# Kernel tuning notes

Measured on AMD Instinct MI355X. Metric: run time of the kernel, lower is better.

## Reference

```python
import jax, jax.numpy as jnp
import numpy as np

B_SZ, L, D, N = 2, 2048, 1024, 16


def setup_inputs() -> dict:
    key = jax.random.key(0)
    ks = jax.random.split(key, 8)
    x = jax.random.normal(ks[0], (B_SZ, L, D), dtype=jnp.float32)
    # torch.nn.Linear params: weight [out, in], bias [out]; y = x @ W.T + b
    s1 = 1.0 / np.sqrt(D)
    W1 = jax.random.uniform(ks[1], (D, D), minval=-s1, maxval=s1, dtype=jnp.float32)
    b1 = jax.random.uniform(ks[2], (D,), minval=-s1, maxval=s1, dtype=jnp.float32)
    W2 = jax.random.uniform(ks[3], (N, D), minval=-s1, maxval=s1, dtype=jnp.float32)
    b2 = jax.random.uniform(ks[4], (N,), minval=-s1, maxval=s1, dtype=jnp.float32)
    W3 = jax.random.uniform(ks[5], (N, D), minval=-s1, maxval=s1, dtype=jnp.float32)
    b3 = jax.random.uniform(ks[6], (N,), minval=-s1, maxval=s1, dtype=jnp.float32)
    # A: xavier_uniform on (D, N)
    lim = np.sqrt(6.0 / (D + N))
    A = jax.random.uniform(ks[7], (D, N), minval=-lim, maxval=lim, dtype=jnp.float32)
    return {"x": x, "W1": W1, "b1": b1, "W2": W2, "b2": b2, "W3": W3, "b3": b3, "A": A}


def reference(x, W1, b1, W2, b2, W3, b3, A):
    # delta = softplus(fc1(x)); B = fc2(x); C = fc3(x)
    delta = jax.nn.softplus(x @ W1.T + b1)          # [b, l, d]
    Bm = x @ W2.T + b2                               # [b, l, n]
    Cm = x @ W3.T + b3                               # [b, l, n]
    # discretization: dB = einsum('bld,bln->bldn', delta, B)
    dB = jnp.einsum('bld,bln->bldn', delta, Bm)      # [b, l, d, n]
    # dA = exp(einsum('bld,dn->bldn', delta, A)) is computed in the source but
    # multiplies a zero-initialized h, so it does not affect the output.
    # h = dA*0 + x[..., None] * dB
    h = x[..., None] * dB                            # [b, l, d, n]
    y = jnp.einsum('bln,bldn->bld', Cm, h)           # [b, l, d]
    return y
```

## Files before the change

kernel.cpp:

```cpp
#include <hip/hip_runtime.h>
#include <hip/hip_bf16.h>
#include <math.h>


typedef __bf16 bf16x8 __attribute__((ext_vector_type(8)));
typedef __bf16 bf16x4 __attribute__((ext_vector_type(4)));
typedef float  f32x4  __attribute__((ext_vector_type(4)));

#define MDIM 4096
#define KDIM 1024
#define NDIM 1024

__device__ __forceinline__ void async16(const void* g, void* l) {
    __builtin_amdgcn_global_load_lds(
        (const __attribute__((address_space(1))) void*)g,
        (__attribute__((address_space(3))) void*)l, 16, 0, 0);
}

__device__ __forceinline__ float softplus_f(float z) {
    return fmaxf(z, 0.f) + log1pf(__expf(-fabsf(z)));
}

#define NX4 ((MDIM * KDIM) / 4)
#define NW4 ((KDIM * NDIM) / 4)
__global__ __launch_bounds__(256)
void convert_kernel(const float* __restrict__ x, const float* __restrict__ W1,
                    __bf16* __restrict__ xb, __bf16* __restrict__ w1b) {
    int i = blockIdx.x * 256 + threadIdx.x;
    if (i < NX4) {
        float4 v = reinterpret_cast<const float4*>(x)[i];
        bf16x4 h = { (__bf16)v.x, (__bf16)v.y, (__bf16)v.z, (__bf16)v.w };
        reinterpret_cast<bf16x4*>(xb)[i] = h;
    } else {
        int j = i - NX4;
        float4 v = reinterpret_cast<const float4*>(W1)[j];
        bf16x4 h = { (__bf16)v.x, (__bf16)v.y, (__bf16)v.z, (__bf16)v.w };
        reinterpret_cast<bf16x4*>(w1b)[j] = h;
    }
}

__global__ __launch_bounds__(256)
void s_kernel_mfma(const __bf16* __restrict__ xb,
                   const float* __restrict__ W2, const float* __restrict__ b2,
                   const float* __restrict__ W3, const float* __restrict__ b3,
                   float* __restrict__ s) {
    __shared__ __align__(16) __bf16 As[64 * 64];
    __shared__ __align__(16) __bf16 Ws[32 * 64];
    const int t = threadIdx.x;
    const int wave = t >> 6, lane = t & 63;
    const int lrow = lane & 15, quad = lane >> 4;
    const int srow = lane >> 3, scol = (lane & 7) * 8;
    const size_t m0 = (size_t)blockIdx.x * 64;

    const int wrow = t >> 3;
    const int wcol = (t & 7) * 8;
    const float* __restrict__ wsrc =
        (wrow < 16) ? (W2 + (size_t)wrow * KDIM) : (W3 + (size_t)(wrow - 16) * KDIM);

    f32x4 acc[2] = {};

    for (int k0 = 0; k0 < KDIM; k0 += 64) {
#pragma unroll
        for (int i = 0; i < 2; ++i) {
            int q = i * 4 + wave;
            int row = 8 * q + srow;
            async16(xb + (m0 + row) * KDIM + k0 + scol, &As[q * 512]);
        }
        {
            float4 v0 = *reinterpret_cast<const float4*>(wsrc + k0 + wcol);
            float4 v1 = *reinterpret_cast<const float4*>(wsrc + k0 + wcol + 4);
            bf16x8 h = { (__bf16)v0.x, (__bf16)v0.y, (__bf16)v0.z, (__bf16)v0.w,
                         (__bf16)v1.x, (__bf16)v1.y, (__bf16)v1.z, (__bf16)v1.w };
            *reinterpret_cast<bf16x8*>(&Ws[wrow * 64 + wcol]) = h;
        }
        __syncthreads();
#pragma unroll
        for (int kk = 0; kk < 64; kk += 32) {
            bf16x8 a = *reinterpret_cast<const bf16x8*>(
                &As[(wave * 16 + lrow) * 64 + kk + quad * 8]);
#pragma unroll
            for (int ni = 0; ni < 2; ++ni) {
                bf16x8 b = *reinterpret_cast<const bf16x8*>(
                    &Ws[(ni * 16 + lrow) * 64 + kk + quad * 8]);
                acc[ni] = __builtin_amdgcn_mfma_f32_16x16x32_bf16(a, b, acc[ni], 0, 0, 0);
            }
        }
        __syncthreads();
    }

    const float b2v = b2[lrow], b3v = b3[lrow];
#pragma unroll
    for (int r = 0; r < 4; ++r) {
        float p = (acc[0][r] + b2v) * (acc[1][r] + b3v);
        p += __shfl_xor(p, 1);
        p += __shfl_xor(p, 2);
        p += __shfl_xor(p, 4);
        p += __shfl_xor(p, 8);
        if (lrow == 0) s[m0 + wave * 16 + quad * 4 + r] = p;
    }
}

#define GBM 128
#define GBN 128
#define GBK 64
__global__ __launch_bounds__(256)
void gemm_bf(const __bf16* __restrict__ xb, const __bf16* __restrict__ w1b,
             const float* __restrict__ x, const float* __restrict__ b1,
             const float* __restrict__ s, float* __restrict__ y) {
    __shared__ __align__(16) __bf16 As[GBM * GBK];
    __shared__ __align__(16) __bf16 Bs[GBN * GBK];
    const int bm = blockIdx.y, bn = blockIdx.x;
    const int t = threadIdx.x;
    const int wave = t >> 6, lane = t & 63;
    const int wm = (wave >> 1) * 64, wn = (wave & 1) * 64;
    const int lrow = lane & 15, quad = lane >> 4;
    const int srow = lane >> 3, scol = (lane & 7) * 8;
    const size_t m0 = (size_t)bm * GBM, n0 = (size_t)bn * GBN;

    f32x4 acc[4][4] = {};

    for (int k0 = 0; k0 < KDIM; k0 += GBK) {
#pragma unroll
        for (int i = 0; i < 4; ++i) {
            int q = i * 4 + wave;
            int row = 8 * q + srow;
            async16(xb  + (m0 + row) * KDIM + k0 + scol, &As[q * 512]);
            async16(w1b + (n0 + row) * KDIM + k0 + scol, &Bs[q * 512]);
        }
        __syncthreads();
#pragma unroll
        for (int kk = 0; kk < GBK; kk += 32) {
            bf16x8 af[4], bfr[4];
#pragma unroll
            for (int mi = 0; mi < 4; ++mi)
                af[mi] = *reinterpret_cast<const bf16x8*>(
                    &As[(wm + mi * 16 + lrow) * GBK + kk + quad * 8]);
#pragma unroll
            for (int ni = 0; ni < 4; ++ni)
                bfr[ni] = *reinterpret_cast<const bf16x8*>(
                    &Bs[(wn + ni * 16 + lrow) * GBK + kk + quad * 8]);
#pragma unroll
            for (int mi = 0; mi < 4; ++mi)
#pragma unroll
                for (int ni = 0; ni < 4; ++ni)
                    acc[mi][ni] = __builtin_amdgcn_mfma_f32_16x16x32_bf16(
                        af[mi], bfr[ni], acc[mi][ni], 0, 0, 0);
        }
        __syncthreads();
    }

#pragma unroll
    for (int ni = 0; ni < 4; ++ni) {
        const size_t gn = n0 + wn + ni * 16 + lrow;
        const float bias = b1[gn];
#pragma unroll
        for (int mi = 0; mi < 4; ++mi) {
#pragma unroll
            for (int r = 0; r < 4; ++r) {
                const size_t gm = m0 + wm + mi * 16 + quad * 4 + r;
                float z = acc[mi][ni][r] + bias;
                y[gm * NDIM + gn] = x[gm * NDIM + gn] * softplus_f(z) * s[gm];
            }
        }
    }
}

__global__ __launch_bounds__(256)
void s_kernel_fb(const float* __restrict__ x,
                 const float* __restrict__ W2, const float* __restrict__ b2,
                 const float* __restrict__ W3, const float* __restrict__ b3,
                 float* __restrict__ s) {
    __shared__ float xs[1024];
    __shared__ float ps[8][32];
    __shared__ float bc[32];
    const int m = blockIdx.x;
    const int t = threadIdx.x;
    reinterpret_cast<float4*>(xs)[t] =
        reinterpret_cast<const float4*>(x + (size_t)m * 1024)[t];
    __syncthreads();
    const int n = t & 15;
    const int mat = (t >> 4) & 1;
    const int seg = t >> 5;
    const float* __restrict__ W = mat ? W3 : W2;
    const float* __restrict__ wr = W + (size_t)n * 1024 + seg * 128;
    const float* __restrict__ xr = xs + seg * 128;
    float p = 0.f;
#pragma unroll
    for (int i = 0; i < 128; i += 4) {
        float4 w4 = *reinterpret_cast<const float4*>(wr + i);
        float4 x4 = *reinterpret_cast<const float4*>(xr + i);
        p += w4.x * x4.x + w4.y * x4.y + w4.z * x4.z + w4.w * x4.w;
    }
    ps[seg][t & 31] = p;
    __syncthreads();
    if (t < 32) {
        float tot = 0.f;
#pragma unroll
        for (int g = 0; g < 8; ++g) tot += ps[g][t];
        tot += (t < 16) ? b2[t] : b3[t - 16];
        bc[t] = tot;
    }
    __syncthreads();
    if (t == 0) {
        float ss = 0.f;
#pragma unroll
        for (int nn = 0; nn < 16; ++nn) ss += bc[nn] * bc[16 + nn];
        s[m] = ss;
    }
}

#define BM 128
#define BN 64
#define BK 64
#define LDK 72
__global__ __launch_bounds__(256)
void gemm_fused_fb(const float* __restrict__ x, const float* __restrict__ W1,
                   const float* __restrict__ b1, const float* __restrict__ s,
                   float* __restrict__ y) {
    __shared__ __align__(16) __bf16 As[BM * LDK];
    __shared__ __align__(16) __bf16 Bs[BN * LDK];
    const int bm = blockIdx.y;
    const int bn = blockIdx.x;
    const int t = threadIdx.x;
    const int wave = t >> 6;
    const int lane = t & 63;
    const int wm = (wave >> 1) * 64;
    const int wn = (wave & 1) * 32;
    const int lrow = lane & 15;
    const int quad = lane >> 4;
    f32x4 acc[4][2] = {};
    const int rbase = t >> 4;
    const int scol = (t & 15) * 4;
    const float* __restrict__ xg = x + (size_t)(bm * BM) * KDIM + scol;
    const float* __restrict__ wg = W1 + (size_t)(bn * BN) * KDIM + scol;
    for (int k0 = 0; k0 < KDIM; k0 += BK) {
#pragma unroll
        for (int rr = 0; rr < 8; ++rr) {
            int row = rr * 16 + rbase;
            float4 v = *reinterpret_cast<const float4*>(xg + (size_t)row * KDIM + k0);
            bf16x4 h = { (__bf16)v.x, (__bf16)v.y, (__bf16)v.z, (__bf16)v.w };
            *reinterpret_cast<bf16x4*>(&As[row * LDK + scol]) = h;
        }
#pragma unroll
        for (int rr = 0; rr < 4; ++rr) {
            int row = rr * 16 + rbase;
            float4 v = *reinterpret_cast<const float4*>(wg + (size_t)row * KDIM + k0);
            bf16x4 h = { (__bf16)v.x, (__bf16)v.y, (__bf16)v.z, (__bf16)v.w };
            *reinterpret_cast<bf16x4*>(&Bs[row * LDK + scol]) = h;
        }
        __syncthreads();
#pragma unroll
        for (int kk = 0; kk < BK; kk += 32) {
            bf16x8 af[4];
            bf16x8 bfr[2];
#pragma unroll
            for (int mi = 0; mi < 4; ++mi)
                af[mi] = *reinterpret_cast<const bf16x8*>(
                    &As[(wm + mi * 16 + lrow) * LDK + kk + quad * 8]);
#pragma unroll
            for (int ni = 0; ni < 2; ++ni)
                bfr[ni] = *reinterpret_cast<const bf16x8*>(
                    &Bs[(wn + ni * 16 + lrow) * LDK + kk + quad * 8]);
#pragma unroll
            for (int mi = 0; mi < 4; ++mi)
#pragma unroll
                for (int ni = 0; ni < 2; ++ni)
                    acc[mi][ni] = __builtin_amdgcn_mfma_f32_16x16x32_bf16(
                        af[mi], bfr[ni], acc[mi][ni], 0, 0, 0);
        }
        __syncthreads();
    }
    const int gmb = bm * BM + wm;
    const int gnb = bn * BN + wn;
#pragma unroll
    for (int ni = 0; ni < 2; ++ni) {
        const int gn = gnb + ni * 16 + lrow;
        const float bias = b1[gn];
#pragma unroll
        for (int mi = 0; mi < 4; ++mi) {
            const int gm0 = gmb + mi * 16 + quad * 4;
#pragma unroll
            for (int r = 0; r < 4; ++r) {
                const int gm = gm0 + r;
                float z = acc[mi][ni][r] + bias;
                y[(size_t)gm * NDIM + gn] =
                    x[(size_t)gm * NDIM + gn] * softplus_f(z) * s[gm];
            }
        }
    }
}

extern "C" void kernel_launch(void* const* d_in, const int* in_sizes, int n_in,
                              void* d_out, int out_size, void* d_ws, size_t ws_size,
                              hipStream_t stream) {
    const float* x  = (const float*)d_in[0];
    const float* W1 = (const float*)d_in[1];
    const float* b1 = (const float*)d_in[2];
    const float* W2 = (const float*)d_in[3];
    const float* b2 = (const float*)d_in[4];
    const float* W3 = (const float*)d_in[5];
    const float* b3 = (const float*)d_in[6];

    float* y = (float*)d_out;

    const size_t XB_BYTES = (size_t)MDIM * KDIM * 2;
    const size_t WB_BYTES = (size_t)NDIM * KDIM * 2;
    const size_t S_BYTES  = (size_t)MDIM * 4;

    if (ws_size >= XB_BYTES + WB_BYTES + S_BYTES) {
        __bf16* xb  = (__bf16*)d_ws;
        __bf16* w1b = (__bf16*)((char*)d_ws + XB_BYTES);
        float*  s   = (float*)((char*)d_ws + XB_BYTES + WB_BYTES);
        convert_kernel<<<dim3((NX4 + NW4) / 256), dim3(256), 0, stream>>>(x, W1, xb, w1b);
        s_kernel_mfma<<<dim3(MDIM / 64), dim3(256), 0, stream>>>(xb, W2, b2, W3, b3, s);
        gemm_bf<<<dim3(NDIM / GBN, MDIM / GBM), dim3(256), 0, stream>>>(xb, w1b, x, b1, s, y);
    } else {
        float* s = (float*)d_ws;
        s_kernel_fb<<<dim3(MDIM), dim3(256), 0, stream>>>(x, W2, b2, W3, b3, s);
        gemm_fused_fb<<<dim3(NDIM / BN, MDIM / BM), dim3(256), 0, stream>>>(x, W1, b1, s, y);
    }
}
```

Measured before the change: 135.4 us.

## Fuse conversion and s-projection into one prep kernel; swizzle LDS and shrink GEMM tile

Result: faster. 114.0 us (-15.8%).

```diff
diff --git a/kernel.cpp b/kernel.cpp
--- a/kernel.cpp
+++ b/kernel.cpp
@@ -21,87 +21,86 @@
     return fmaxf(z, 0.f) + log1pf(__expf(-fabsf(z)));
 }
 
-#define NX4 ((MDIM * KDIM) / 4)
-#define NW4 ((KDIM * NDIM) / 4)
 __global__ __launch_bounds__(256)
-void convert_kernel(const float* __restrict__ x, const float* __restrict__ W1,
-                    __bf16* __restrict__ xb, __bf16* __restrict__ w1b) {
-    int i = blockIdx.x * 256 + threadIdx.x;
-    if (i < NX4) {
-        float4 v = reinterpret_cast<const float4*>(x)[i];
-        bf16x4 h = { (__bf16)v.x, (__bf16)v.y, (__bf16)v.z, (__bf16)v.w };
-        reinterpret_cast<bf16x4*>(xb)[i] = h;
-    } else {
-        int j = i - NX4;
-        float4 v = reinterpret_cast<const float4*>(W1)[j];
-        bf16x4 h = { (__bf16)v.x, (__bf16)v.y, (__bf16)v.z, (__bf16)v.w };
-        reinterpret_cast<bf16x4*>(w1b)[j] = h;
-    }
-}
-
-__global__ __launch_bounds__(256)
-void s_kernel_mfma(const __bf16* __restrict__ xb,
-                   const float* __restrict__ W2, const float* __restrict__ b2,
-                   const float* __restrict__ W3, const float* __restrict__ b3,
-                   float* __restrict__ s) {
-    __shared__ __align__(16) __bf16 As[64 * 64];
-    __shared__ __align__(16) __bf16 Ws[32 * 64];
+void prep_kernel(const float* __restrict__ x, const float* __restrict__ W1,
+                 const float* __restrict__ W2, const float* __restrict__ b2,
+                 const float* __restrict__ W3, const float* __restrict__ b3,
+                 __bf16* __restrict__ xb, __bf16* __restrict__ w1b,
+                 float* __restrict__ s) {
+    __shared__ __align__(16) __bf16 xs[16 * 1032];
+    __shared__ float red[4][2][16][16];
     const int t = threadIdx.x;
     const int wave = t >> 6, lane = t & 63;
     const int lrow = lane & 15, quad = lane >> 4;
-    const int srow = lane >> 3, scol = (lane & 7) * 8;
-    const size_t m0 = (size_t)blockIdx.x * 64;
-
-    const int wrow = t >> 3;
-    const int wcol = (t & 7) * 8;
-    const float* __restrict__ wsrc =
-        (wrow < 16) ? (W2 + (size_t)wrow * KDIM) : (W3 + (size_t)(wrow - 16) * KDIM);
+    const size_t m0 = (size_t)blockIdx.x * 16;
+
+    {
+        const float4* src = reinterpret_cast<const float4*>(W1) + (size_t)blockIdx.x * 1024;
+        bf16x4* dst = reinterpret_cast<bf16x4*>(w1b) + (size_t)blockIdx.x * 1024;
+#pragma unroll
+        for (int i = 0; i < 4; ++i) {
+            float4 v = src[i * 256 + t];
+            bf16x4 h = { (__bf16)v.x, (__bf16)v.y, (__bf16)v.z, (__bf16)v.w };
+            dst[i * 256 + t] = h;
+        }
+    }
+
+#pragma unroll
+    for (int i = 0; i < 16; ++i) {
+        float4 v = *reinterpret_cast<const float4*>(x + (m0 + i) * KDIM + t * 4);
+        bf16x4 h = { (__bf16)v.x, (__bf16)v.y, (__bf16)v.z, (__bf16)v.w };
+        *reinterpret_cast<bf16x4*>(&xs[i * 1032 + t * 4]) = h;
+        *reinterpret_cast<bf16x4*>(xb + (m0 + i) * KDIM + t * 4) = h;
+    }
+    __syncthreads();
 
     f32x4 acc[2] = {};
-
-    for (int k0 = 0; k0 < KDIM; k0 += 64) {
-#pragma unroll
-        for (int i = 0; i < 2; ++i) {
-            int q = i * 4 + wave;
-            int row = 8 * q + srow;
-            async16(xb + (m0 + row) * KDIM + k0 + scol, &As[q * 512]);
-        }
+    const int wk0 = wave * 256;
+#pragma unroll
+    for (int ks = 0; ks < 256; ks += 32) {
+        bf16x8 a = *reinterpret_cast<const bf16x8*>(
+            &xs[lrow * 1032 + wk0 + ks + quad * 8]);
         {
-            float4 v0 = *reinterpret_cast<const float4*>(wsrc + k0 + wcol);
-            float4 v1 = *reinterpret_cast<const float4*>(wsrc + k0 + wcol + 4);
-            bf16x8 h = { (__bf16)v0.x, (__bf16)v0.y, (__bf16)v0.z, (__bf16)v0.w,
+            const float* wp = W2 + (size_t)lrow * KDIM + wk0 + ks + quad * 8;
+            float4 v0 = *reinterpret_cast<const float4*>(wp);
+            float4 v1 = *reinterpret_cast<const float4*>(wp + 4);
+            bf16x8 b = { (__bf16)v0.x, (__bf16)v0.y, (__bf16)v0.z, (__bf16)v0.w,
                          (__bf16)v1.x, (__bf16)v1.y, (__bf16)v1.z, (__bf16)v1.w };
-            *reinterpret_cast<bf16x8*>(&Ws[wrow * 64 + wcol]) = h;
-        }
-        __syncthreads();
-#pragma unroll
-        for (int kk = 0; kk < 64; kk += 32) {
-            bf16x8 a = *reinterpret_cast<const bf16x8*>(
-                &As[(wave * 16 + lrow) * 64 + kk + quad * 8]);
-#pragma unroll
-            for (int ni = 0; ni < 2; ++ni) {
-                bf16x8 b = *reinterpret_cast<const bf16x8*>(
-                    &Ws[(ni * 16 + lrow) * 64 + kk + quad * 8]);
-                acc[ni] = __builtin_amdgcn_mfma_f32_16x16x32_bf16(a, b, acc[ni], 0, 0, 0);
-            }
-        }
-        __syncthreads();
-    }
-
-    const float b2v = b2[lrow], b3v = b3[lrow];
+            acc[0] = __builtin_amdgcn_mfma_f32_16x16x32_bf16(a, b, acc[0], 0, 0, 0);
+        }
+        {
+            const float* wp = W3 + (size_t)lrow * KDIM + wk0 + ks + quad * 8;
+            float4 v0 = *reinterpret_cast<const float4*>(wp);
+            float4 v1 = *reinterpret_cast<const float4*>(wp + 4);
+            bf16x8 b = { (__bf16)v0.x, (__bf16)v0.y, (__bf16)v0.z, (__bf16)v0.w,
+                         (__bf16)v1.x, (__bf16)v1.y, (__bf16)v1.z, (__bf16)v1.w };
+            acc[1] = __builtin_amdgcn_mfma_f32_16x16x32_bf16(a, b, acc[1], 0, 0, 0);
+        }
+    }
 #pragma unroll
     for (int r = 0; r < 4; ++r) {
-        float p = (acc[0][r] + b2v) * (acc[1][r] + b3v);
+        red[wave][0][quad * 4 + r][lrow] = acc[0][r];
+        red[wave][1][quad * 4 + r][lrow] = acc[1][r];
+    }
+    __syncthreads();
+
+    {
+        const int row = t >> 4, n = t & 15;
+        float Bv = red[0][0][row][n] + red[1][0][row][n]
+                 + red[2][0][row][n] + red[3][0][row][n] + b2[n];
+        float Cv = red[0][1][row][n] + red[1][1][row][n]
+                 + red[2][1][row][n] + red[3][1][row][n] + b3[n];
+        float p = Bv * Cv;
         p += __shfl_xor(p, 1);
         p += __shfl_xor(p, 2);
         p += __shfl_xor(p, 4);
         p += __shfl_xor(p, 8);
-        if (lrow == 0) s[m0 + wave * 16 + quad * 4 + r] = p;
+        if (n == 0) s[m0 + row] = p;
     }
 }
 
 #define GBM 128
-#define GBN 128
+#define GBN 64
 #define GBK 64
 __global__ __launch_bounds__(256)
 void gemm_bf(const __bf16* __restrict__ xb, const __bf16* __restrict__ w1b,
@@ -112,37 +111,49 @@
     const int bm = blockIdx.y, bn = blockIdx.x;
     const int t = threadIdx.x;
     const int wave = t >> 6, lane = t & 63;
-    const int wm = (wave >> 1) * 64, wn = (wave & 1) * 64;
+    const int wm = (wave >> 1) * 64, wn = (wave & 1) * 32;
     const int lrow = lane & 15, quad = lane >> 4;
-    const int srow = lane >> 3, scol = (lane & 7) * 8;
+    const int srow = lane >> 3;
+    const int scol = ((lane & 7) ^ srow) * 8;
     const size_t m0 = (size_t)bm * GBM, n0 = (size_t)bn * GBN;
 
-    f32x4 acc[4][4] = {};
+    f32x4 acc[4][2] = {};
 
     for (int k0 = 0; k0 < KDIM; k0 += GBK) {
 #pragma unroll
         for (int i = 0; i < 4; ++i) {
             int q = i * 4 + wave;
             int row = 8 * q + srow;
-            async16(xb  + (m0 + row) * KDIM + k0 + scol, &As[q * 512]);
+            async16(xb + (m0 + row) * KDIM + k0 + scol, &As[q * 512]);
+        }
+#pragma unroll
+        for (int i = 0; i < 2; ++i) {
+            int q = i * 4 + wave;
+            int row = 8 * q + srow;
             async16(w1b + (n0 + row) * KDIM + k0 + scol, &Bs[q * 512]);
         }
         __syncthreads();
+
 #pragma unroll
         for (int kk = 0; kk < GBK; kk += 32) {
-            bf16x8 af[4], bfr[4];
+            const int cg = (kk >> 3) + quad;
+            bf16x8 af[4], bfr[2];
+#pragma unroll
+            for (int mi = 0; mi < 4; ++mi) {
+                int row = wm + mi * 16 + lrow;
+                af[mi] = *reinterpret_cast<const bf16x8*>(
+                    &As[row * 64 + ((cg ^ (row & 7)) << 3)]);
+            }
+#pragma unroll
+            for (int ni = 0; ni < 2; ++ni) {
+                int row = wn + ni * 16 + lrow;
+                bfr[ni] = *reinterpret_cast<const bf16x8*>(
+                    &Bs[row * 64 + ((cg ^ (row & 7)) << 3)]);
+            }
 #pragma unroll
             for (int mi = 0; mi < 4; ++mi)
-                af[mi] = *reinterpret_cast<const bf16x8*>(
-                    &As[(wm + mi * 16 + lrow) * GBK + kk + quad * 8]);
-#pragma unroll
-            for (int ni = 0; ni < 4; ++ni)
-                bfr[ni] = *reinterpret_cast<const bf16x8*>(
-                    &Bs[(wn + ni * 16 + lrow) * GBK + kk + quad * 8]);
-#pragma unroll
-            for (int mi = 0; mi < 4; ++mi)
-#pragma unroll
-                for (int ni = 0; ni < 4; ++ni)
+#pragma unroll
+                for (int ni = 0; ni < 2; ++ni)
                     acc[mi][ni] = __builtin_amdgcn_mfma_f32_16x16x32_bf16(
                         af[mi], bfr[ni], acc[mi][ni], 0, 0, 0);
         }
@@ -150,7 +161,7 @@
     }
 
 #pragma unroll
-    for (int ni = 0; ni < 4; ++ni) {
+    for (int ni = 0; ni < 2; ++ni) {
         const size_t gn = n0 + wn + ni * 16 + lrow;
         const float bias = b1[gn];
 #pragma unroll
@@ -311,9 +322,10 @@
         __bf16* xb  = (__bf16*)d_ws;
         __bf16* w1b = (__bf16*)((char*)d_ws + XB_BYTES);
         float*  s   = (float*)((char*)d_ws + XB_BYTES + WB_BYTES);
-        convert_kernel<<<dim3((NX4 + NW4) / 256), dim3(256), 0, stream>>>(x, W1, xb, w1b);
-        s_kernel_mfma<<<dim3(MDIM / 64), dim3(256), 0, stream>>>(xb, W2, b2, W3, b3, s);
-        gemm_bf<<<dim3(NDIM / GBN, MDIM / GBM), dim3(256), 0, stream>>>(xb, w1b, x, b1, s, y);
+        prep_kernel<<<dim3(MDIM / 16), dim3(256), 0, stream>>>(
+            x, W1, W2, b2, W3, b3, xb, w1b, s);
+        gemm_bf<<<dim3(NDIM / GBN, MDIM / GBM), dim3(256), 0, stream>>>(
+            xb, w1b, x, b1, s, y);
     } else {
         float* s = (float*)d_ws;
         s_kernel_fb<<<dim3(MDIM), dim3(256), 0, stream>>>(x, W2, b2, W3, b3, s);
```
